# Kernel tuning notes

Measured on AMD Instinct MI355X. Metric: run time of the kernel, lower is better.

## Reference

```python
import jax, jax.numpy as jnp
import numpy as np

EPS = 1e-12  # torch F.normalize clamp_min eps


def _linear_interp(t, M):
    # PyTorch F.interpolate(mode='linear', align_corners=False) along last axis.
    L = t.shape[-1]
    src = (jnp.arange(M, dtype=t.dtype) + 0.5) * (L / M) - 0.5
    src = jnp.maximum(src, 0.0)
    i0 = jnp.minimum(jnp.floor(src).astype(jnp.int32), L - 1)
    i1 = jnp.minimum(i0 + 1, L - 1)
    frac = src - i0.astype(t.dtype)
    return t[..., i0] * (1.0 - frac) + t[..., i1] * frac


def _l2norm(t):
    n = jnp.linalg.norm(t, axis=-1, keepdims=True)
    return t / jnp.maximum(n, EPS)


def setup_inputs() -> dict:
    key = jax.random.key(0)
    ks = jax.random.split(key, 6)
    b, dim, m = 4, 512, 4096
    h = w = 64
    heads = 8
    s = 0.02
    return {
        "x": jax.random.normal(ks[0], (b, dim, m), dtype=jnp.float32),
        "y": jax.random.normal(ks[1], (b, dim, h, w), dtype=jnp.float32),
        "temperature": jnp.ones((heads, 1, 1), dtype=jnp.float32),
        "w_kv": jax.random.normal(ks[2], (2 * dim, dim), dtype=jnp.float32) * s,
        "w_q": jax.random.normal(ks[3], (dim, dim), dtype=jnp.float32) * s,
        "w_dw": jax.random.normal(ks[4], (dim, dim, 3, 3), dtype=jnp.float32) * s,
        "w_out": jax.random.normal(ks[5], (dim, dim), dtype=jnp.float32) * s,
    }


def reference(x, y, temperature, w_kv, w_q, w_dw, w_out):
    b, c, m = x.shape
    heads = temperature.shape[0]
    hd = c // heads

    # kv = Conv1d(dim, 2*dim, k=1)(x); split into k, v
    kv = jnp.einsum('bcm,oc->bom', x, w_kv)
    k, v = jnp.split(kv, 2, axis=1)

    # q = dwconv3x3(Conv2d 1x1(y)) -> flatten -> linear-resize to m
    q = jnp.einsum('bchw,oc->bohw', y, w_q)
    q = jax.lax.conv_general_dilated(
        q, w_dw, window_strides=(1, 1), padding=[(1, 1), (1, 1)],
        dimension_numbers=('NCHW', 'OIHW', 'NCHW'))
    q = q.reshape(b, c, -1)
    q = _linear_interp(q, m)

    # split heads: [b, head, c', m]
    q = _l2norm(q.reshape(b, heads, hd, m))
    k = _l2norm(k.reshape(b, heads, hd, m))
    v = v.reshape(b, heads, hd, m)

    # channel-wise attention: [b, head, c', c']
    attn = jnp.einsum('bhcm,bhdm->bhcd', q, k) * temperature
    attn = jax.nn.softmax(attn, axis=-1)
    out = jnp.einsum('bhcd,bhdm->bhcm', attn, v).reshape(b, c, m)

    # project_out: Conv1d k=1
    return jnp.einsum('bcm,oc->bom', out, w_out)
```

## Files before the change

### kernel.cpp

```cpp
#include <hip/hip_runtime.h>
#include <hip/hip_bf16.h>
#include <math.h>

typedef float f32x4 __attribute__((ext_vector_type(4)));
typedef int   i32x4 __attribute__((ext_vector_type(4)));
typedef short s16x8 __attribute__((ext_vector_type(8)));

#define NB 4
#define NC 512
#define NM 4096
#define NHEADS 8

#define GLDS16(src, dst) __builtin_amdgcn_global_load_lds( \
    (const __attribute__((address_space(1))) void*)(src),  \
    (__attribute__((address_space(3))) void*)(dst), 16, 0, 0)

__global__ __launch_bounds__(256) void prep_tr(
    const float* __restrict__ wdw, const float* __restrict__ wkv,
    const float* __restrict__ wq,
    const float* __restrict__ x, const float* __restrict__ y,
    __hip_bfloat16* __restrict__ Wr, __hip_bfloat16* __restrict__ wkvB,
    __hip_bfloat16* __restrict__ wqT, __hip_bfloat16* __restrict__ zeropad,
    float* __restrict__ norms,
    __hip_bfloat16* __restrict__ xT, __hip_bfloat16* __restrict__ yT)
{
  __shared__ __hip_bfloat16 tile[64][68];
  const int bx = blockIdx.x;
  if (bx < 4113) {
    long idx = (long)bx * 256 + threadIdx.x;
    if (idx < 262144) {
      const float* s = wdw + idx * 9;
      #pragma unroll
      for (int r = 0; r < 9; r++)
        Wr[(long)r * 262144 + idx] = __float2bfloat16(s[r]);
    } else if (idx < 786432) {
      long j = idx - 262144;
      wkvB[j] = __float2bfloat16(wkv[j]);
    } else if (idx < 1048576) {
      long j = idx - 786432;
      int c = (int)(j >> 9), cp = (int)(j & 511);
      wqT[j] = __float2bfloat16(wq[(long)cp * 512 + c]);
    } else if (idx < 1048704) {
      zeropad[idx - 1048576] = __float2bfloat16(0.f);
    } else if (idx < 1052800) {
      norms[idx - 1048704] = 0.f;
    }
  } else {
    const int rem = bx - 4113;
    const int z = rem >> 9;
    const int tm = (rem & 63) * 64, tc = ((rem >> 6) & 7) * 64;
    const float* src = ((z < 4) ? x : y) + (long)(z & 3) * ((long)NC * NM);
    __hip_bfloat16* dst = (z < 4 ? xT : yT) + (long)(z & 3) * ((long)NC * NM);
    int tx4 = threadIdx.x & 15, trow = threadIdx.x >> 4;
    #pragma unroll
    for (int p = 0; p < 4; p++) {
      int crow = trow + p * 16;
      f32x4 v = *(const f32x4*)&src[(long)(tc + crow) * NM + tm + tx4 * 4];
      #pragma unroll
      for (int t = 0; t < 4; t++) tile[crow][tx4 * 4 + t] = __float2bfloat16(v[t]);
    }
    __syncthreads();
    #pragma unroll
    for (int p = 0; p < 4; p++) {
      int mrow = trow + p * 16;
      union { ushort4 u4; unsigned short u[4]; } o;
      #pragma unroll
      for (int t = 0; t < 4; t++)
        o.u[t] = *(const unsigned short*)&tile[tx4 * 4 + t][mrow];
      *(ushort4*)&dst[(long)(tm + mrow) * NC + tc + tx4 * 4] = o.u4;
    }
  }
}

__global__ __launch_bounds__(256) void gemm_bt(
    const __hip_bfloat16* __restrict__ Aall, long sA,
    const __hip_bfloat16* __restrict__ Ball, long sB,
    __hip_bfloat16* __restrict__ Cball, float* __restrict__ Cfall, long sC,
    int M, int N, int Kd, int outMode)
{
  const __hip_bfloat16* A = Aall + (long)blockIdx.z * sA;
  const __hip_bfloat16* B = Ball + (long)blockIdx.z * sB;
  const int m0 = blockIdx.y * 128, n0 = blockIdx.x * 128;
  __shared__ __hip_bfloat16 As[128 * 32];
  __shared__ __hip_bfloat16 Bs[128 * 32];
  const int tid = threadIdx.x;
  const int wid = tid >> 6, lane = tid & 63;
  const int wm = (wid >> 1) * 64, wn = (wid & 1) * 64;
  const int quad = lane >> 4, l16 = lane & 15;
  const int srow = wid * 32 + (lane >> 2);
  const int scol = (lane & 3) * 8;
  f32x4 acc[4][4] = {};
  for (int k0 = 0; k0 < Kd; k0 += 32) {
    __syncthreads();
    #pragma unroll
    for (int t = 0; t < 2; t++) {
      GLDS16(A + (long)(m0 + srow + t * 16) * Kd + k0 + scol,
             As + (wid * 32 + t * 16) * 32);
      GLDS16(B + (long)(n0 + srow + t * 16) * Kd + k0 + scol,
             Bs + (wid * 32 + t * 16) * 32);
    }
    __builtin_amdgcn_s_waitcnt(0);
    __syncthreads();
    s16x8 bfr[4];
    #pragma unroll
    for (int j = 0; j < 4; j++)
      bfr[j] = *(const s16x8*)(&Bs[(wn + j * 16 + l16) * 32 + quad * 8]);
    #pragma unroll
    for (int i = 0; i < 4; i++) {
      s16x8 af = *(const s16x8*)(&As[(wm + i * 16 + l16) * 32 + quad * 8]);
      #pragma unroll
      for (int j = 0; j < 4; j++)
        acc[i][j] = __builtin_amdgcn_mfma_f32_16x16x32_bf16(af, bfr[j], acc[i][j], 0, 0, 0);
    }
  }
  if (outMode == 1) {
    float* C = Cfall + (long)blockIdx.z * sC;
    #pragma unroll
    for (int i = 0; i < 4; i++)
      #pragma unroll
      for (int j = 0; j < 4; j++) {
        int rbase = m0 + wm + i * 16 + quad * 4;
        int col = n0 + wn + j * 16 + l16;
        #pragma unroll
        for (int r = 0; r < 4; r++)
          C[(long)(rbase + r) * N + col] = acc[i][j][r];
      }
  } else if (outMode == 2) {
    __hip_bfloat16* C = Cball;
    const int rt = blockIdx.z;
    #pragma unroll
    for (int i = 0; i < 4; i++)
      #pragma unroll
      for (int j = 0; j < 4; j++) {
        int obase = m0 + wm + i * 16 + quad * 4;
        int col = n0 + wn + j * 16 + l16;
        #pragma unroll
        for (int r = 0; r < 4; r++) {
          int o = obase + r;
          long idx = ((((long)(rt * 32 + (o >> 4)) * 16 + (col >> 5)) << 9)
                      + ((col >> 3) & 3) * 128 + (o & 15) * 8 + (col & 7));
          C[idx] = __float2bfloat16(acc[i][j][r]);
        }
      }
  } else {
    __hip_bfloat16* C = Cball + (long)blockIdx.z * sC;
    #pragma unroll
    for (int i = 0; i < 4; i++)
      #pragma unroll
      for (int j = 0; j < 4; j++) {
        int rbase = m0 + wm + i * 16 + quad * 4;
        int col = n0 + wn + j * 16 + l16;
        #pragma unroll
        for (int r = 0; r < 4; r++)
          C[(long)(rbase + r) * N + col] = __float2bfloat16(acc[i][j][r]);
      }
  }
}

__global__ __launch_bounds__(256) void gemm_kv(
    const __hip_bfloat16* __restrict__ wkvB,
    const __hip_bfloat16* __restrict__ xT,
    __hip_bfloat16* __restrict__ Kb,
    __hip_bfloat16* __restrict__ Vt,
    float* __restrict__ knorm2)
{
  const int z = blockIdx.z;
  const int b = z & 3;
  const bool kmode = (z < 4);
  const long S = (long)NM * NC;
  const __hip_bfloat16* A = kmode ? wkvB : (xT + b * S);
  const __hip_bfloat16* B = kmode ? (xT + b * S) : (wkvB + 262144);
  __hip_bfloat16* C = kmode ? (Kb + b * S) : (Vt + b * S);
  const int m0 = (kmode ? blockIdx.y : blockIdx.x) * 128;
  const int n0 = (kmode ? blockIdx.x : blockIdx.y) * 128;
  const int N = kmode ? NM : NC;
  __shared__ __hip_bfloat16 As[128 * 32];
  __shared__ __hip_bfloat16 Bs[128 * 32];
  const int tid = threadIdx.x;
  const int wid = tid >> 6, lane = tid & 63;
  const int wm = (wid >> 1) * 64, wn = (wid & 1) * 64;
  const int quad = lane >> 4, l16 = lane & 15;
  const int srow = wid * 32 + (lane >> 2);
  const int scol = (lane & 3) * 8;
  f32x4 acc[4][4] = {};
  for (int k0 = 0; k0 < NC; k0 += 32) {
    __syncthreads();
    #pragma unroll
    for (int t = 0; t < 2; t++) {
      GLDS16(A + (long)(m0 + srow + t * 16) * NC + k0 + scol,
             As + (wid * 32 + t * 16) * 32);
      GLDS16(B + (long)(n0 + srow + t * 16) * NC + k0 + scol,
             Bs + (wid * 32 + t * 16) * 32);
    }
    __builtin_amdgcn_s_waitcnt(0);
    __syncthreads();
    s16x8 bfr[4];
    #pragma unroll
    for (int j = 0; j < 4; j++)
      bfr[j] = *(const s16x8*)(&Bs[(wn + j * 16 + l16) * 32 + quad * 8]);
    #pragma unroll
    for (int i = 0; i < 4; i++) {
      s16x8 af = *(const s16x8*)(&As[(wm + i * 16 + l16) * 32 + quad * 8]);
      #pragma unroll
      for (int j = 0; j < 4; j++)
        acc[i][j] = __builtin_amdgcn_mfma_f32_16x16x32_bf16(af, bfr[j], acc[i][j], 0, 0, 0);
    }
  }
  #pragma unroll
  for (int i = 0; i < 4; i++)
    #pragma unroll
    for (int j = 0; j < 4; j++) {
      int rbase = m0 + wm + i * 16 + quad * 4;
      int col = n0 + wn + j * 16 + l16;
      #pragma unroll
      for (int r = 0; r < 4; r++)
        C[(long)(rbase + r) * N + col] = __float2bfloat16(acc[i][j][r]);
    }
  if (kmode) {
    #pragma unroll
    for (int i = 0; i < 4; i++) {
      int rbase = m0 + wm + i * 16 + quad * 4;
      #pragma unroll
      for (int r = 0; r < 4; r++) {
        float s = 0.f;
        #pragma unroll
        for (int j = 0; j < 4; j++) s += acc[i][j][r] * acc[i][j][r];
        s += __shfl_xor(s, 1); s += __shfl_xor(s, 2);
        s += __shfl_xor(s, 4); s += __shfl_xor(s, 8);
        if (l16 == 0) atomicAdd(&knorm2[b * 512 + rbase + r], s);
      }
    }
  }
}

__global__ __launch_bounds__(256) void conv3x3(
    const __hip_bfloat16* __restrict__ Wp,
    const __hip_bfloat16* __restrict__ yT,
    const __hip_bfloat16* __restrict__ zeropad,
    __hip_bfloat16* __restrict__ q2,
    float* __restrict__ qnorm2)
{
  const int b = blockIdx.z;
  const int n0 = blockIdx.x * 128;
  const int m0 = blockIdx.y * 128;
  __shared__ __hip_bfloat16 As2[2][24 * 512];
  __shared__ __hip_bfloat16 Bs2[2][256 * 32];
  const int tid = threadIdx.x;
  const int wid = tid >> 6, lane = tid & 63;
  const int wm = (wid >> 1) * 64, wn = (wid & 1) * 64;
  const int quad = lane >> 4, l16 = lane & 15;
  const int lrow = lane >> 2;
  const int h0 = n0 >> 6;
  const int mb0b = m0 >> 4;
  const int mwl = wm >> 4;
  const __hip_bfloat16* yb = yT + (long)b * NM * NC;
  f32x4 acc[4][4] = {};
  const s16x8 zero8 = {0, 0, 0, 0, 0, 0, 0, 0};

  const int sq = ((lane & 3) ^ ((lane >> 3) & 3)) * 8;

  int addr0[3][4];
  unsigned vbits = 0;
  #pragma unroll
  for (int t = 0; t < 3; t++) {
    #pragma unroll
    for (int j = 0; j < 4; j++) {
      int nl = wn + j * 16 + l16;
      int wq_ = nl & 63, hr = nl >> 6;
      int wp = wq_ + t - 1;
      unsigned v = ((unsigned)wp) < 64u;
      int p = v ? (hr * 64 + wp) : 0;
      addr0[t][j] = p * 32 + ((quad ^ ((p >> 1) & 3)) * 8);
      vbits |= v << (t * 4 + j);
    }
  }


  #pragma unroll
  for (int k = 0; k < 6; k++) {
    int f = wid * 6 + k;
    GLDS16(Wp + (((long)(((f >> 3)) * 32 + mb0b + (f & 7)) * 16 + 0) << 9) + lane * 8,
           &As2[0][f * 512]);
  }
  #pragma unroll
  for (int t = 0; t < 4; t++) {
    int pr = wid * 64 + t * 16 + lrow;
    int hw = (h0 - 1) * 64 + pr;
    const __hip_bfloat16* src = (((unsigned)hw) < (unsigned)NM)
        ? (yb + (long)hw * NC + sq) : zeropad;
    GLDS16(src, &Bs2[0][(wid * 64 + t * 16) * 32]);
  }
  __builtin_amdgcn_s_waitcnt(0);
  __syncthreads();

  for (int icb = 0; icb < 16; icb++) {
    const __hip_bfloat16* Bcur = &Bs2[icb & 1][0];
    #pragma unroll
    for (int g = 0; g < 3; g++) {
      const int cb = (icb ^ g) & 1;
      const __hip_bfloat16* Acur = &As2[cb][0];
      __hip_bfloat16* Anxt = (__hip_bfloat16*)&As2[cb ^ 1][0];
      if (icb < 15 || g < 2) {
        const int gn = (g == 2) ? 0 : g + 1;
        const int icbn = (g == 2) ? icb + 1 : icb;
        #pragma unroll
        for (int k = 0; k < 6; k++) {
          int f = wid * 6 + k;
          GLDS16(Wp + (((long)((gn * 3 + (f >> 3)) * 32 + mb0b + (f & 7)) * 16 + icbn) << 9) + lane * 8,
                 Anxt + f * 512);
        }
      }
      if (g == 1 && icb < 15) {
        __hip_bfloat16* Bnxt = (__hip_bfloat16*)&Bs2[(icb & 1) ^ 1][0];
        #pragma unroll
        for (int t = 0; t < 4; t++) {
          int pr = wid * 64 + t * 16 + lrow;
          int hw = (h0 - 1) * 64 + pr;
          const __hip_bfloat16* src = (((unsigned)hw) < (unsigned)NM)
              ? (yb + (long)hw * NC + (icb + 1) * 32 + sq) : zeropad;
          GLDS16(src, Bnxt + (wid * 64 + t * 16) * 32);
        }
      }
      #pragma unroll
      for (int t = 0; t < 3; t++) {
        s16x8 bfr[4];
        #pragma unroll
        for (int j = 0; j < 4; j++) {
          s16x8 tt = *(const s16x8*)(&Bcur[addr0[t][j] + g * 2048]);
          bfr[j] = ((vbits >> (t * 4 + j)) & 1u) ? tt : zero8;
        }
        #pragma unroll
        for (int i = 0; i < 4; i++) {
          s16x8 af = *(const s16x8*)(&Acur[(t * 8 + mwl + i) * 512 + lane * 8]);
          #pragma unroll
          for (int j = 0; j < 4; j++)
            acc[i][j] = __builtin_amdgcn_mfma_f32_16x16x32_bf16(af, bfr[j], acc[i][j], 0, 0, 0);
        }
      }
      __builtin_amdgcn_s_waitcnt(0);
      __syncthreads();
    }
  }

  __hip_bfloat16* Cb = q2 + (long)b * NC * NM;
  #pragma unroll
  for (int i = 0; i < 4; i++)
    #pragma unroll
    for (int j = 0; j < 4; j++) {
      int rbase = m0 + wm + i * 16 + quad * 4;
      int col = n0 + wn + j * 16 + l16;
      #pragma unroll
      for (int r = 0; r < 4; r++)
        Cb[(long)(rbase + r) * NM + col] = __float2bfloat16(acc[i][j][r]);
    }
  #pragma unroll
  for (int i = 0; i < 4; i++) {
    int rbase = m0 + wm + i * 16 + quad * 4;
    #pragma unroll
    for (int r = 0; r < 4; r++) {
      float s = 0.f;
      #pragma unroll
      for (int j = 0; j < 4; j++) s += acc[i][j][r] * acc[i][j][r];
      s += __shfl_xor(s, 1); s += __shfl_xor(s, 2);
      s += __shfl_xor(s, 4); s += __shfl_xor(s, 8);
      if (l16 == 0) atomicAdd(&qnorm2[b * 512 + rbase + r], s);
    }
  }
}

__global__ __launch_bounds__(256) void attn_g(
    const __hip_bfloat16* __restrict__ q2, const __hip_bfloat16* __restrict__ Kb,
    float* __restrict__ Gpart)
{
  const int mc = blockIdx.x, h = blockIdx.y, b = blockIdx.z;
  const __hip_bfloat16* qrow = q2 + ((long)b * NC + h * 64) * NM + mc * 512;
  const __hip_bfloat16* krow = Kb + ((long)b * NC + h * 64) * NM + mc * 512;
  __shared__ __hip_bfloat16 Qs[64 * 40];
  __shared__ __hip_bfloat16 Ks[64 * 40];
  const int tid = threadIdx.x;
  const int wid = tid >> 6, lane = tid & 63;
  const int wc = (wid >> 1) * 32, wd = (wid & 1) * 32;
  const int quad = lane >> 4, l16 = lane & 15;
  const int srow = tid >> 2, scol = (tid & 3) * 8;
  f32x4 acc[2][2] = {};
  for (int k0 = 0; k0 < 512; k0 += 32) {
    __syncthreads();
    *(i32x4*)(&Qs[srow * 40 + scol]) = *(const i32x4*)(&qrow[(long)srow * NM + k0 + scol]);
    *(i32x4*)(&Ks[srow * 40 + scol]) = *(const i32x4*)(&krow[(long)srow * NM + k0 + scol]);
    __syncthreads();
    s16x8 bfr[2];
    #pragma unroll
    for (int j = 0; j < 2; j++)
      bfr[j] = *(const s16x8*)(&Ks[(wd + j * 16 + l16) * 40 + quad * 8]);
    #pragma unroll
    for (int i = 0; i < 2; i++) {
      s16x8 af = *(const s16x8*)(&Qs[(wc + i * 16 + l16) * 40 + quad * 8]);
      #pragma unroll
      for (int j = 0; j < 2; j++)
        acc[i][j] = __builtin_amdgcn_mfma_f32_16x16x32_bf16(af, bfr[j], acc[i][j], 0, 0, 0);
    }
  }
  float* gp = Gpart + ((long)((b * 8 + h) * 8 + mc)) * 4096;
  #pragma unroll
  for (int i = 0; i < 2; i++)
    #pragma unroll
    for (int j = 0; j < 2; j++)
      #pragma unroll
      for (int r = 0; r < 4; r++)
        gp[(wc + i * 16 + quad * 4 + r) * 64 + wd + j * 16 + l16] = acc[i][j][r];
}

__global__ __launch_bounds__(256) void softmax_wa(
    const float* __restrict__ Gpart, const float* __restrict__ qnorm2,
    const float* __restrict__ knorm2, const float* __restrict__ temp,
    const float* __restrict__ wout, __hip_bfloat16* __restrict__ Wa)
{
  const int oc = blockIdx.x, h = blockIdx.y, b = blockIdx.z;
  __shared__ float G[64][64];
  __shared__ float Wt[64][65];
  const int tid = threadIdx.x;
  const float tv = temp[h];
  for (int e = tid; e < 4096; e += 256) {
    float s = 0.f;
    #pragma unroll
    for (int p = 0; p < 8; p++)
      s += Gpart[((long)((b * 8 + h) * 8 + p)) * 4096 + e];
    int c = e >> 6, d = e & 63;
    float qn = fmaxf(sqrtf(qnorm2[b * 512 + h * 64 + c]), 1e-12f);
    float kn = fmaxf(sqrtf(knorm2[b * 512 + h * 64 + d]), 1e-12f);
    G[c][d] = s * tv / (qn * kn);
    Wt[c][d] = wout[(long)(oc * 64 + c) * 512 + h * 64 + d];
  }
  __syncthreads();
  int row = tid >> 2, s4 = tid & 3;
  float mx = -1e30f;
  for (int d = s4; d < 64; d += 4) mx = fmaxf(mx, G[row][d]);
  mx = fmaxf(mx, __shfl_xor(mx, 1));
  mx = fmaxf(mx, __shfl_xor(mx, 2));
  float sum = 0.f;
  for (int d = s4; d < 64; d += 4) { float e = __expf(G[row][d] - mx); G[row][d] = e; sum += e; }
  sum += __shfl_xor(sum, 1);
  sum += __shfl_xor(sum, 2);
  float inv = 1.f / sum;
  for (int d = s4; d < 64; d += 4) G[row][d] *= inv;
  __syncthreads();
  int d = tid & 63, og = tid >> 6;
  #pragma unroll
  for (int k2 = 0; k2 < 16; k2++) {
    int o = og * 16 + k2;
    float s = 0.f;
    #pragma unroll 8
    for (int c = 0; c < 64; c++) s += Wt[o][c] * G[c][d];
    Wa[((long)b * 512 + oc * 64 + o) * 512 + h * 64 + d] = __float2bfloat16(s);
  }
}

extern "C" void kernel_launch(void* const* d_in, const int* in_sizes, int n_in,
                              void* d_out, int out_size, void* d_ws, size_t ws_size,
                              hipStream_t stream) {
  const float* x    = (const float*)d_in[0];
  const float* y    = (const float*)d_in[1];
  const float* temp = (const float*)d_in[2];
  const float* wkv  = (const float*)d_in[3];
  const float* wq   = (const float*)d_in[4];
  const float* wdw  = (const float*)d_in[5];
  const float* wout = (const float*)d_in[6];
  float* out = (float*)d_out;

  char* ws = (char*)d_ws;
  const long TEN = 16777216;
  __hip_bfloat16* xT  = (__hip_bfloat16*)(ws);
  __hip_bfloat16* q2  = xT;
  __hip_bfloat16* yT  = (__hip_bfloat16*)(ws + TEN);
  float* Gpart        = (float*)(ws + TEN);
  __hip_bfloat16* Wa  = (__hip_bfloat16*)(ws + TEN + 4718592);
  __hip_bfloat16* Kb  = (__hip_bfloat16*)(ws + 2 * TEN);
  __hip_bfloat16* Vt  = (__hip_bfloat16*)(ws + 3 * TEN);
  __hip_bfloat16* Wfold = (__hip_bfloat16*)(ws + 4 * TEN);
  __hip_bfloat16* Wr    = (__hip_bfloat16*)(ws + 4 * TEN + 4718592);
  __hip_bfloat16* wkvB  = (__hip_bfloat16*)(ws + 4 * TEN + 9437184);
  __hip_bfloat16* wqT   = (__hip_bfloat16*)(ws + 4 * TEN + 10485760);
  __hip_bfloat16* zeropad = (__hip_bfloat16*)(ws + 4 * TEN + 11010048);
  float* norms          = (float*)(ws + 4 * TEN + 11010304);
  float* knorm2 = norms;
  float* qnorm2 = norms + 2048;

  const long S = (long)4096 * 512;
  const long S2 = (long)512 * 512;
  dim3 blk(256);

  prep_tr<<<dim3(8209), blk, 0, stream>>>(wdw, wkv, wq, x, y,
                                          Wr, wkvB, wqT, zeropad, norms, xT, yT);
  gemm_bt<<<dim3(4, 4, 9), blk, 0, stream>>>(Wr, S2, wqT, 0L, Wfold, nullptr, 0L, 512, 512, 512, 2);
  gemm_kv<<<dim3(32, 4, 8), blk, 0, stream>>>(wkvB, xT, Kb, Vt, knorm2);
  conv3x3<<<dim3(32, 4, 4), blk, 0, stream>>>(Wfold, yT, zeropad, q2, qnorm2);
  attn_g<<<dim3(8, 8, 4), blk, 0, stream>>>(q2, Kb, Gpart);
  softmax_wa<<<dim3(8, 8, 4), blk, 0, stream>>>(Gpart, qnorm2, knorm2, temp, wout, Wa);
  gemm_bt<<<dim3(32, 4, 4), blk, 0, stream>>>(Wa, S2, Vt, S, nullptr, out, S, 512, 4096, 512, 1);
  (void)in_sizes; (void)n_in; (void)out_size; (void)ws_size;
}
```

Before: 297.9 us.

## Pipeline conv3x3 weight loads per tap with triple-buffered LDS and partial vmcnt waits

The conv3x3 GEMM main loop now runs per tap (9 per channel block) instead of per group of 3 taps. A triple-buffered A tile is prefetched two taps ahead, the B tile is issued mid-iteration, and full waitcnt(0) plus syncthreads is replaced by partial vmcnt waits plus a raw barrier. The aim is to keep global-to-LDS loads in flight across barriers and to cut LDS footprint. The cost is more barriers per block, and the correctness of the hand-counted vmcnt thresholds is fragile.

```diff
diff --git a/kernel.cpp b/kernel.cpp
--- a/kernel.cpp
+++ b/kernel.cpp
@@ -14,6 +14,10 @@
 #define GLDS16(src, dst) __builtin_amdgcn_global_load_lds( \
     (const __attribute__((address_space(1))) void*)(src),  \
     (__attribute__((address_space(3))) void*)(dst), 16, 0, 0)
+
+#define WAITVM0 asm volatile("s_waitcnt vmcnt(0)" ::: "memory")
+#define WAITVM2 asm volatile("s_waitcnt vmcnt(2)" ::: "memory")
+#define WAITVM6 asm volatile("s_waitcnt vmcnt(6)" ::: "memory")
 
 __global__ __launch_bounds__(256) void prep_tr(
     const float* __restrict__ wdw, const float* __restrict__ wkv,
@@ -243,7 +247,7 @@
   const int b = blockIdx.z;
   const int n0 = blockIdx.x * 128;
   const int m0 = blockIdx.y * 128;
-  __shared__ __hip_bfloat16 As2[2][24 * 512];
+  __shared__ __hip_bfloat16 As3[3][8 * 512];
   __shared__ __hip_bfloat16 Bs2[2][256 * 32];
   const int tid = threadIdx.x;
   const int wid = tid >> 6, lane = tid & 63;
@@ -275,54 +279,51 @@
     }
   }
 
-
-  #pragma unroll
-  for (int k = 0; k < 6; k++) {
-    int f = wid * 6 + k;
-    GLDS16(Wp + (((long)(((f >> 3)) * 32 + mb0b + (f & 7)) * 16 + 0) << 9) + lane * 8,
-           &As2[0][f * 512]);
-  }
-  #pragma unroll
-  for (int t = 0; t < 4; t++) {
-    int pr = wid * 64 + t * 16 + lrow;
-    int hw = (h0 - 1) * 64 + pr;
-    const __hip_bfloat16* src = (((unsigned)hw) < (unsigned)NM)
-        ? (yb + (long)hw * NC + sq) : zeropad;
-    GLDS16(src, &Bs2[0][(wid * 64 + t * 16) * 32]);
-  }
-  __builtin_amdgcn_s_waitcnt(0);
-  __syncthreads();
+  const int f0 = wid * 2, f1 = wid * 2 + 1;
+
+#define AISSUE(slot_, rt_, icb_) { \
+    GLDS16(Wp + (((long)((rt_) * 32 + mb0b + f0) * 16 + (icb_)) << 9) + lane * 8, \
+           &As3[slot_][f0 * 512]); \
+    GLDS16(Wp + (((long)((rt_) * 32 + mb0b + f1) * 16 + (icb_)) << 9) + lane * 8, \
+           &As3[slot_][f1 * 512]); }
+
+#define BISSUE(icb_, bufidx_) { \
+    _Pragma("unroll") \
+    for (int t_ = 0; t_ < 4; t_++) { \
+      int pr = wid * 64 + t_ * 16 + lrow; \
+      int hw = (h0 - 1) * 64 + pr; \
+      const __hip_bfloat16* src = (((unsigned)hw) < (unsigned)NM) \
+          ? (yb + (long)hw * NC + (icb_) * 32 + sq) : zeropad; \
+      GLDS16(src, &Bs2[bufidx_][(wid * 64 + t_ * 16) * 32]); \
+    } }
+
+  BISSUE(0, 0);
+  AISSUE(0, 0, 0);
+  AISSUE(1, 1, 0);
 
   for (int icb = 0; icb < 16; icb++) {
     const __hip_bfloat16* Bcur = &Bs2[icb & 1][0];
     #pragma unroll
-    for (int g = 0; g < 3; g++) {
-      const int cb = (icb ^ g) & 1;
-      const __hip_bfloat16* Acur = &As2[cb][0];
-      __hip_bfloat16* Anxt = (__hip_bfloat16*)&As2[cb ^ 1][0];
-      if (icb < 15 || g < 2) {
-        const int gn = (g == 2) ? 0 : g + 1;
-        const int icbn = (g == 2) ? icb + 1 : icb;
-        #pragma unroll
-        for (int k = 0; k < 6; k++) {
-          int f = wid * 6 + k;
-          GLDS16(Wp + (((long)((gn * 3 + (f >> 3)) * 32 + mb0b + (f & 7)) * 16 + icbn) << 9) + lane * 8,
-                 Anxt + f * 512);
-        }
-      }
-      if (g == 1 && icb < 15) {
-        __hip_bfloat16* Bnxt = (__hip_bfloat16*)&Bs2[(icb & 1) ^ 1][0];
-        #pragma unroll
-        for (int t = 0; t < 4; t++) {
-          int pr = wid * 64 + t * 16 + lrow;
-          int hw = (h0 - 1) * 64 + pr;
-          const __hip_bfloat16* src = (((unsigned)hw) < (unsigned)NM)
-              ? (yb + (long)hw * NC + (icb + 1) * 32 + sq) : zeropad;
-          GLDS16(src, Bnxt + (wid * 64 + t * 16) * 32);
-        }
-      }
-      #pragma unroll
-      for (int t = 0; t < 3; t++) {
+    for (int tap = 0; tap < 9; tap++) {
+      if (tap == 5 || tap == 6) {
+        if (icb < 15) { WAITVM6; } else { WAITVM2; }
+      } else if (tap == 8) {
+        if (icb == 15) { WAITVM0; } else { WAITVM2; }
+      } else {
+        WAITVM2;
+      }
+      asm volatile("" ::: "memory");
+      __builtin_amdgcn_s_barrier();
+      asm volatile("" ::: "memory");
+      if (icb < 15 || tap < 7) {
+        const int rt2 = (tap + 2) % 9;
+        const int sl2 = (tap + 2) % 3;
+        const int icb2 = icb + ((tap + 2) / 9);
+        AISSUE(sl2, rt2, icb2);
+      }
+      if (tap == 4 && icb < 15) BISSUE(icb + 1, (icb & 1) ^ 1);
+      {
+        const int g = tap / 3, t = tap % 3;
         s16x8 bfr[4];
         #pragma unroll
         for (int j = 0; j < 4; j++) {
@@ -331,16 +332,16 @@
         }
         #pragma unroll
         for (int i = 0; i < 4; i++) {
-          s16x8 af = *(const s16x8*)(&Acur[(t * 8 + mwl + i) * 512 + lane * 8]);
+          s16x8 af = *(const s16x8*)(&As3[tap % 3][(mwl + i) * 512 + lane * 8]);
           #pragma unroll
           for (int j = 0; j < 4; j++)
             acc[i][j] = __builtin_amdgcn_mfma_f32_16x16x32_bf16(af, bfr[j], acc[i][j], 0, 0, 0);
         }
       }
-      __builtin_amdgcn_s_waitcnt(0);
-      __syncthreads();
-    }
-  }
+    }
+  }
+#undef AISSUE
+#undef BISSUE
 
   __hip_bfloat16* Cb = q2 + (long)b * NC * NM;
   #pragma unroll
```

New measurement: 312.1 us. 4.8% more time.
